# Optimization experiments

Hardware: AMD Instinct MI355X
Metric: run time of the kernel (lower is better)

Reference implementation:

```python
import jax, jax.numpy as jnp
import numpy as np

N, C, T, V = 128, 256, 48, 25
CR = C // 16
SEG = 3
BN_EPS = 1e-5


def setup_inputs() -> dict:
    key = jax.random.key(0)
    ks = jax.random.split(key, 8)
    s = lambda k, shape: jax.random.normal(k, shape, dtype=jnp.float32) * 0.05
    return {
        "x": jax.random.normal(ks[0], (N, C, T, V), dtype=jnp.float32),
        "w_sq": s(ks[1], (CR, C)),   # me_squeeze 1x1 conv weight [out,in]
        "b_sq": s(ks[2], (CR,)),
        "gamma": jnp.ones((CR,), jnp.float32),   # BN weight
        "beta": jnp.zeros((CR,), jnp.float32),   # BN bias
        "rmean": jnp.zeros((CR,), jnp.float32),  # BN running mean
        "rvar": jnp.ones((CR,), jnp.float32),    # BN running var
        "w_c1": s(ks[3], (CR, CR)),  # me_conv1 1x1 conv weight
        "b_c1": s(ks[4], (CR,)),
        "w_ex": s(ks[5], (C, CR)),   # me_expand 1x1 conv weight
        "b_ex": s(ks[6], (C,)),
    }


def reference(x, w_sq, b_sq, gamma, beta, rmean, rvar, w_c1, b_c1, w_ex, b_ex):
    n, c, t, v = x.shape
    nb = (n * t) // SEG
    cr = w_sq.shape[0]
    # 1x1 squeeze conv + BatchNorm (eval mode, running stats) -> [n, cr, t, v]
    y = jnp.einsum('nctv,rc->nrtv', x, w_sq) + b_sq[None, :, None, None]
    scale = gamma / jnp.sqrt(rvar + BN_EPS)
    y = y * scale[None, :, None, None] + (beta - rmean * scale)[None, :, None, None]
    # 1x1 conv on squeezed features (shifted branch)
    y1 = jnp.einsum('nrtv,sr->nstv', y, w_c1) + b_c1[None, :, None, None]
    # regroup consecutive frames into segments of SEG along time: (n*t) -> (nb, SEG)
    yseg = y.transpose(0, 2, 1, 3).reshape(nb, SEG, cr, v)
    y1seg = y1.transpose(0, 2, 1, 3).reshape(nb, SEG, cr, v)
    # temporal difference: conv(frame k+1) - frame k, zero-pad last frame of each segment
    diff = y1seg[:, 1:] - yseg[:, :SEG - 1]                    # [nb, SEG-1, cr, v]
    diff = jnp.pad(diff, ((0, 0), (0, 1), (0, 0), (0, 0)))     # [nb, SEG, cr, v]
    x_me = diff.reshape(n, t, cr, v).transpose(0, 2, 1, 3)     # [n, cr, t, v]
    # adaptive avg pool over joints (v -> 1), expand conv, sigmoid gate
    m = jnp.mean(x_me, axis=-1, keepdims=True)                 # [n, cr, t, 1]
    gate = jax.nn.sigmoid(jnp.einsum('nrtu,cr->nctu', m, w_ex) + b_ex[None, :, None, None])
    return x * gate
```

## Files before the change

### kernel.cpp

```cpp
#include <hip/hip_runtime.h>

typedef float v4f __attribute__((ext_vector_type(4)));

__global__ __launch_bounds__(512, 4) void k_fused8(
    const float* __restrict__ x,
    const float* __restrict__ wsq, const float* __restrict__ bsq,
    const float* __restrict__ gamma, const float* __restrict__ beta,
    const float* __restrict__ rmean, const float* __restrict__ rvar,
    const float* __restrict__ wc1, const float* __restrict__ bc1,
    const float* __restrict__ wex, const float* __restrict__ bex,
    float* __restrict__ out)
{
    __shared__ v4f   buf[2][16 * 77];
    __shared__ float xb[12 * 256];
    __shared__ float wsqL[256 * 17];
    __shared__ float ybn[192], y1[192], mv[192];

    const int tid = threadIdx.x;
    const unsigned bid = blockIdx.x;
    const unsigned o = (bid & 7u) * 64u + (bid >> 3);
    const unsigned n = o >> 2;
    const unsigned q = o & 3u;

    const v4f* x4 = (const v4f*)x + (size_t)n * 76800u + q * 75u;
    v4f*       o4 = (v4f*)out     + (size_t)n * 76800u + q * 75u;

    float* gsb = (float*)buf;

    float acc = 0.f;

    auto stage = [&](int cg, v4f* dst) {
        const int pt = tid - 384;
        v4f tmp[10];
        #pragma unroll
        for (int i = 0; i < 10; ++i) {
            int s = i * 128 + pt;
            int sc = (s < 1200) ? s : 1199;
            int c = sc / 75, k = sc - c * 75;
            tmp[i] = x4[(cg * 16 + c) * 300 + k];
        }
        #pragma unroll
        for (int i = 0; i < 10; ++i) {
            int s = i * 128 + pt;
            int sc = (s < 1200) ? s : 1199;
            int c = sc / 75, k = sc - c * 75;
            dst[c * 77 + k] = tmp[i];
        }
    };
    auto reduceC = [&](int cg) {
        int t = tid >> 4, cl = tid & 15;
        const float* bp = (const float*)&buf[cg & 1][cl * 77] + t * 25;
        float s = 0.f;
        #pragma unroll
        for (int v = 0; v < 25; ++v) s += bp[v];
        xb[t * 256 + cg * 16 + cl] = s;
    };
    auto accumB1 = [&](int cg) {
        int u = tid - 192, t = u >> 4, r = u & 15;
        #pragma unroll
        for (int i = 0; i < 16; ++i) {
            int c = cg * 16 + i;
            acc += xb[t * 256 + c] * wsqL[c * 17 + r];
        }
    };

    #pragma unroll
    for (int it = 0; it < 8; ++it) {
        int j = it * 512 + tid;
        wsqL[(j & 255) * 17 + (j >> 8)] = wsq[j];
    }
    if (tid >= 384) stage(0, buf[0]);
    __syncthreads();

    for (int i = 0; i < 16; ++i) {
        if (tid >= 384) { if (i < 15) stage(i + 1, buf[(i + 1) & 1]); }
        else if (tid < 192) reduceC(i);
        else if (i > 0) accumB1(i - 1);
        __syncthreads();
    }

    if (tid >= 192 && tid < 384) {
        accumB1(15);
        int u = tid - 192, r = u & 15;
        float sc = gamma[r] * rsqrtf(rvar[r] + 1e-5f);
        ybn[u] = acc * (0.04f * sc) + (bsq[r] * sc + beta[r] - rmean[r] * sc);
    }
    __syncthreads();
    if (tid < 192) {
        int t = tid >> 4, s = tid & 15;
        float a = bc1[s];
        #pragma unroll
        for (int r = 0; r < 16; ++r) a += ybn[t * 16 + r] * wc1[s * 16 + r];
        y1[tid] = a;
    }
    __syncthreads();
    if (tid < 192) {
        int t = tid >> 4;
        mv[tid] = ((t % 3) < 2) ? (y1[tid + 16] - ybn[tid]) : 0.f;
    }
    __syncthreads();
    {
        int c = tid & 255, half = tid >> 8;
        float wexr[16];
        #pragma unroll
        for (int r = 0; r < 16; ++r) wexr[r] = wex[c * 16 + r];
        float be = bex[c];
        #pragma unroll
        for (int t = half * 6; t < half * 6 + 6; ++t) {
            float a = be;
            #pragma unroll
            for (int r = 0; r < 16; ++r) a += mv[t * 16 + r] * wexr[r];
            gsb[c * 12 + t] = 1.f / (1.f + expf(-a));
        }
    }
    __syncthreads();

    #pragma unroll 4
    for (int it = 0; it < 38; ++it) {
        int j = it * 512 + tid;
        if (j < 19200) {
            unsigned c = ((unsigned)j * 55926u) >> 22;
            int k = j - (int)c * 75;
            v4f v = x4[c * 300 + k];
            int m0  = k * 4;
            int t0  = (m0 * 41) >> 10;
            int t3  = ((m0 + 3) * 41) >> 10;
            int rem = m0 - t0 * 25;
            float g0 = gsb[c * 12 + t0];
            float g3 = gsb[c * 12 + t3];
            v4f ov;
            ov.x = v.x * g0;
            ov.y = v.y * ((rem + 1 < 25) ? g0 : g3);
            ov.z = v.z * ((rem + 2 < 25) ? g0 : g3);
            ov.w = v.w * ((rem + 3 < 25) ? g0 : g3);
            __builtin_nontemporal_store(ov, &o4[c * 300 + k]);
        }
    }
}

extern "C" void kernel_launch(void* const* d_in, const int* in_sizes, int n_in,
                              void* d_out, int out_size, void* d_ws, size_t ws_size,
                              hipStream_t stream) {
    const float* x     = (const float*)d_in[0];
    const float* wsq   = (const float*)d_in[1];
    const float* bsq   = (const float*)d_in[2];
    const float* gamma = (const float*)d_in[3];
    const float* beta  = (const float*)d_in[4];
    const float* rmean = (const float*)d_in[5];
    const float* rvar  = (const float*)d_in[6];
    const float* wc1   = (const float*)d_in[7];
    const float* bc1   = (const float*)d_in[8];
    const float* wex   = (const float*)d_in[9];
    const float* bex   = (const float*)d_in[10];

    k_fused8<<<512, 512, 0, stream>>>(x, wsq, bsq, gamma, beta,
                                      rmean, rvar, wc1, bc1, wex, bex,
                                      (float*)d_out);
}
```

Measured before the change: 77.02 us.

## Spread x staging across all threads with register double-buffered prefetch

Every thread now loads x tiles into LDS, instead of a dedicated 128-thread producer group. Loads are issued two channel-groups ahead into alternating register buffers, and a custom barrier waits only on LDS counters, so global loads stay in flight across barriers. The LDS tile layout drops the 77-wide padding for contiguous 300-float channel rows, and the xb row stride is padded to 260. This is meant to raise memory-level parallelism in the reduction phase. It costs more registers and may change LDS bank-conflict behaviour.

New measurement: 77.57 us. No clear change (+0.7%).

```diff
diff --git a/kernel.cpp b/kernel.cpp
--- a/kernel.cpp
+++ b/kernel.cpp
@@ -2,7 +2,7 @@
 
 typedef float v4f __attribute__((ext_vector_type(4)));
 
-__global__ __launch_bounds__(512, 4) void k_fused8(
+__global__ __launch_bounds__(512, 4) void k_fused9(
     const float* __restrict__ x,
     const float* __restrict__ wsq, const float* __restrict__ bsq,
     const float* __restrict__ gamma, const float* __restrict__ beta,
@@ -11,8 +11,8 @@
     const float* __restrict__ wex, const float* __restrict__ bex,
     float* __restrict__ out)
 {
-    __shared__ v4f   buf[2][16 * 77];
-    __shared__ float xb[12 * 256];
+    __shared__ v4f   buf[2][1200];
+    __shared__ float xb[12 * 260];
     __shared__ float wsqL[256 * 17];
     __shared__ float ybn[192], y1[192], mv[192];
 
@@ -24,59 +24,67 @@
 
     const v4f* x4 = (const v4f*)x + (size_t)n * 76800u + q * 75u;
     v4f*       o4 = (v4f*)out     + (size_t)n * 76800u + q * 75u;
-
     float* gsb = (float*)buf;
 
     float acc = 0.f;
+    v4f tA[3], tB[3];
 
-    auto stage = [&](int cg, v4f* dst) {
-        const int pt = tid - 384;
-        v4f tmp[10];
+    auto issue = [&](int cg, v4f* t3) {
         #pragma unroll
-        for (int i = 0; i < 10; ++i) {
-            int s = i * 128 + pt;
-            int sc = (s < 1200) ? s : 1199;
-            int c = sc / 75, k = sc - c * 75;
-            tmp[i] = x4[(cg * 16 + c) * 300 + k];
+        for (int it = 0; it < 3; ++it) {
+            int s = it * 512 + tid;
+            if (s < 1200) {
+                int c = s / 75, k = s - c * 75;
+                t3[it] = x4[(cg * 16 + c) * 300 + k];
+            }
         }
+    };
+    auto writeL = [&](int cg, const v4f* t3) {
         #pragma unroll
-        for (int i = 0; i < 10; ++i) {
-            int s = i * 128 + pt;
-            int sc = (s < 1200) ? s : 1199;
-            int c = sc / 75, k = sc - c * 75;
-            dst[c * 77 + k] = tmp[i];
+        for (int it = 0; it < 3; ++it) {
+            int s = it * 512 + tid;
+            if (s < 1200) buf[cg & 1][s] = t3[it];
         }
     };
     auto reduceC = [&](int cg) {
         int t = tid >> 4, cl = tid & 15;
-        const float* bp = (const float*)&buf[cg & 1][cl * 77] + t * 25;
+        const float* bp = (const float*)buf[cg & 1] + cl * 300 + t * 25;
         float s = 0.f;
         #pragma unroll
         for (int v = 0; v < 25; ++v) s += bp[v];
-        xb[t * 256 + cg * 16 + cl] = s;
+        xb[t * 260 + cg * 16 + cl] = s;
     };
     auto accumB1 = [&](int cg) {
         int u = tid - 192, t = u >> 4, r = u & 15;
         #pragma unroll
-        for (int i = 0; i < 16; ++i) {
-            int c = cg * 16 + i;
-            acc += xb[t * 256 + c] * wsqL[c * 17 + r];
+        for (int i2 = 0; i2 < 16; ++i2) {
+            int c = cg * 16 + i2;
+            acc += xb[t * 260 + c] * wsqL[c * 17 + r];
         }
     };
+    auto bar = [&]() {
+        asm volatile("s_waitcnt lgkmcnt(0)" ::: "memory");
+        __builtin_amdgcn_s_barrier();
+        __builtin_amdgcn_sched_barrier(0);
+    };
 
+    issue(0, tA);
     #pragma unroll
     for (int it = 0; it < 8; ++it) {
         int j = it * 512 + tid;
         wsqL[(j & 255) * 17 + (j >> 8)] = wsq[j];
     }
-    if (tid >= 384) stage(0, buf[0]);
-    __syncthreads();
+    writeL(0, tA);
+    issue(1, tB);
+    bar();
 
+    #pragma unroll
     for (int i = 0; i < 16; ++i) {
-        if (tid >= 384) { if (i < 15) stage(i + 1, buf[(i + 1) & 1]); }
-        else if (tid < 192) reduceC(i);
-        else if (i > 0) accumB1(i - 1);
-        __syncthreads();
+        if (i < 15) writeL(i + 1, (i & 1) ? tA : tB);
+        if (i < 14) issue(i + 2, (i & 1) ? tB : tA);
+        if (tid < 192) reduceC(i);
+        else if (tid < 384 && i > 0) accumB1(i - 1);
+        bar();
     }
 
     if (tid >= 192 && tid < 384) {
@@ -153,7 +161,7 @@
     const float* wex   = (const float*)d_in[9];
     const float* bex   = (const float*)d_in[10];
 
-    k_fused8<<<512, 512, 0, stream>>>(x, wsq, bsq, gamma, beta,
+    k_fused9<<<512, 512, 0, stream>>>(x, wsq, bsq, gamma, beta,
                                       rmean, rvar, wc1, bc1, wex, bex,
                                       (float*)d_out);
 }
```

## Replace block-wide staged reduction with per-warp double-buffered channel loads

Applied to the files above, without the earlier changes.

The block-wide pipeline, where 128 threads staged x tiles and the other threads reduced and accumulated with a __syncthreads every channel group, is replaced. Now each of the 8 wavefronts loads its own 32 channels with register double-buffering and reduces them over joints into LDS without any block barriers. The squeeze matvec then runs afterwards as a split-K dot product over 384 threads, followed by a pairwise combine. This is meant to remove the 16 block-wide barriers and put all threads to work on loading x. The cost is more registers, less overlap between the load and the matvec, and shared-memory buffers that are reused for weights and gates.

Result: slower. 79.49 us (+3.2%).

```diff
diff --git a/kernel.cpp b/kernel.cpp
--- a/kernel.cpp
+++ b/kernel.cpp
@@ -2,7 +2,7 @@
 
 typedef float v4f __attribute__((ext_vector_type(4)));
 
-__global__ __launch_bounds__(512, 4) void k_fused8(
+__global__ __launch_bounds__(512, 4) void k_fused11(
     const float* __restrict__ x,
     const float* __restrict__ wsq, const float* __restrict__ bsq,
     const float* __restrict__ gamma, const float* __restrict__ beta,
@@ -11,12 +11,17 @@
     const float* __restrict__ wex, const float* __restrict__ bex,
     float* __restrict__ out)
 {
-    __shared__ v4f   buf[2][16 * 77];
-    __shared__ float xb[12 * 256];
-    __shared__ float wsqL[256 * 17];
+    __shared__ v4f   wb[8][2][152];
+    __shared__ float xb[12 * 260];
+    __shared__ float part[384];
     __shared__ float ybn[192], y1[192], mv[192];
 
+    float* wsqL = (float*)wb;
+    float* gs   = (float*)wb + 4352;
+
     const int tid = threadIdx.x;
+    const int w   = tid >> 6;
+    const int ln  = tid & 63;
     const unsigned bid = blockIdx.x;
     const unsigned o = (bid & 7u) * 64u + (bid >> 3);
     const unsigned n = o >> 2;
@@ -25,65 +30,74 @@
     const v4f* x4 = (const v4f*)x + (size_t)n * 76800u + q * 75u;
     v4f*       o4 = (v4f*)out     + (size_t)n * 76800u + q * 75u;
 
-    float* gsb = (float*)buf;
+    const int crBase = w * 32;
 
-    float acc = 0.f;
-
-    auto stage = [&](int cg, v4f* dst) {
-        const int pt = tid - 384;
-        v4f tmp[10];
+    v4f sA[3], sB[3];
+    auto issueW = [&](int rnd, v4f* st) {
+        int cr = crBase + rnd * 2;
         #pragma unroll
-        for (int i = 0; i < 10; ++i) {
-            int s = i * 128 + pt;
-            int sc = (s < 1200) ? s : 1199;
-            int c = sc / 75, k = sc - c * 75;
-            tmp[i] = x4[(cg * 16 + c) * 300 + k];
-        }
-        #pragma unroll
-        for (int i = 0; i < 10; ++i) {
-            int s = i * 128 + pt;
-            int sc = (s < 1200) ? s : 1199;
-            int c = sc / 75, k = sc - c * 75;
-            dst[c * 77 + k] = tmp[i];
+        for (int qq = 0; qq < 3; ++qq) {
+            int s = qq * 64 + ln;
+            if (s < 150) {
+                int c = cr + (s >= 75 ? 1 : 0);
+                int k = (s >= 75) ? s - 75 : s;
+                st[qq] = x4[c * 300 + k];
+            }
         }
     };
-    auto reduceC = [&](int cg) {
-        int t = tid >> 4, cl = tid & 15;
-        const float* bp = (const float*)&buf[cg & 1][cl * 77] + t * 25;
-        float s = 0.f;
+    auto writeW = [&](int rnd, const v4f* st) {
+        v4f* dst = wb[w][rnd & 1];
         #pragma unroll
-        for (int v = 0; v < 25; ++v) s += bp[v];
-        xb[t * 256 + cg * 16 + cl] = s;
-    };
-    auto accumB1 = [&](int cg) {
-        int u = tid - 192, t = u >> 4, r = u & 15;
-        #pragma unroll
-        for (int i = 0; i < 16; ++i) {
-            int c = cg * 16 + i;
-            acc += xb[t * 256 + c] * wsqL[c * 17 + r];
+        for (int qq = 0; qq < 3; ++qq) {
+            int s = qq * 64 + ln;
+            if (s < 150) dst[s] = st[qq];
         }
     };
+    auto reduceW = [&](int rnd) {
+        if (ln < 24) {
+            int co = ln / 12, t = ln - co * 12;
+            const float* bp = (const float*)wb[w][rnd & 1] + co * 300 + t * 25;
+            float s = 0.f;
+            #pragma unroll
+            for (int v = 0; v < 25; ++v) s += bp[v];
+            xb[t * 260 + crBase + rnd * 2 + co] = s;
+        }
+    };
+
+    issueW(0, sA);
+    issueW(1, sB);
+    #pragma unroll
+    for (int r = 0; r < 16; r += 2) {
+        writeW(r, sA);
+        if (r + 2 < 16) issueW(r + 2, sA);
+        reduceW(r);
+        writeW(r + 1, sB);
+        if (r + 3 < 16) issueW(r + 3, sB);
+        reduceW(r + 1);
+    }
+    __syncthreads();
 
     #pragma unroll
     for (int it = 0; it < 8; ++it) {
         int j = it * 512 + tid;
         wsqL[(j & 255) * 17 + (j >> 8)] = wsq[j];
     }
-    if (tid >= 384) stage(0, buf[0]);
     __syncthreads();
 
-    for (int i = 0; i < 16; ++i) {
-        if (tid >= 384) { if (i < 15) stage(i + 1, buf[(i + 1) & 1]); }
-        else if (tid < 192) reduceC(i);
-        else if (i > 0) accumB1(i - 1);
-        __syncthreads();
+    if (tid < 384) {
+        int t = tid >> 5, rh = tid & 31, r = rh >> 1, hh = rh & 1;
+        float acc = 0.f;
+        #pragma unroll 8
+        for (int i = 0; i < 128; ++i)
+            acc += xb[t * 260 + hh * 128 + i] * wsqL[(hh * 128 + i) * 17 + r];
+        part[tid] = acc;
     }
-
-    if (tid >= 192 && tid < 384) {
-        accumB1(15);
-        int u = tid - 192, r = u & 15;
+    __syncthreads();
+    if (tid < 192) {
+        int t = tid >> 4, r = tid & 15;
+        float acc = part[t * 32 + r * 2] + part[t * 32 + r * 2 + 1];
         float sc = gamma[r] * rsqrtf(rvar[r] + 1e-5f);
-        ybn[u] = acc * (0.04f * sc) + (bsq[r] * sc + beta[r] - rmean[r] * sc);
+        ybn[tid] = acc * (0.04f * sc) + (bsq[r] * sc + beta[r] - rmean[r] * sc);
     }
     __syncthreads();
     if (tid < 192) {
@@ -110,7 +124,7 @@
             float a = be;
             #pragma unroll
             for (int r = 0; r < 16; ++r) a += mv[t * 16 + r] * wexr[r];
-            gsb[c * 12 + t] = 1.f / (1.f + expf(-a));
+            gs[c * 12 + t] = 1.f / (1.f + expf(-a));
         }
     }
     __syncthreads();
@@ -126,8 +140,8 @@
             int t0  = (m0 * 41) >> 10;
             int t3  = ((m0 + 3) * 41) >> 10;
             int rem = m0 - t0 * 25;
-            float g0 = gsb[c * 12 + t0];
-            float g3 = gsb[c * 12 + t3];
+            float g0 = gs[c * 12 + t0];
+            float g3 = gs[c * 12 + t3];
             v4f ov;
             ov.x = v.x * g0;
             ov.y = v.y * ((rem + 1 < 25) ? g0 : g3);
@@ -153,7 +167,7 @@
     const float* wex   = (const float*)d_in[9];
     const float* bex   = (const float*)d_in[10];
 
-    k_fused8<<<512, 512, 0, stream>>>(x, wsq, bsq, gamma, beta,
-                                      rmean, rvar, wc1, bc1, wex, bex,
-                                      (float*)d_out);
+    k_fused11<<<512, 512, 0, stream>>>(x, wsq, bsq, gamma, beta,
+                                       rmean, rvar, wc1, bc1, wex, bex,
+                                       (float*)d_out);
 }
```
